# Optimization experiments

Hardware: AMD Instinct MI355X
Metric: run time of the kernel (lower is better)

The kernel has to match this reference:

```python
import jax, jax.numpy as jnp
import numpy as np

D_MODEL = 1024
N_HEADS = 16
HEAD_DIM = D_MODEL // N_HEADS


def setup_inputs() -> dict:
    key = jax.random.key(0)
    ks = jax.random.split(key, 5)
    B, L = 4, 2048
    x = jax.random.normal(ks[0], (B, L, D_MODEL), dtype=jnp.float32)
    s = 1.0 / np.sqrt(D_MODEL)
    W_qkv = jax.random.normal(ks[1], (D_MODEL, 3 * D_MODEL), dtype=jnp.float32) * s
    b_qkv = jnp.zeros((3 * D_MODEL,), dtype=jnp.float32)
    W_out = jax.random.normal(ks[2], (D_MODEL, D_MODEL), dtype=jnp.float32) * s
    b_out = jnp.zeros((D_MODEL,), dtype=jnp.float32)
    return {"x": x, "W_qkv": W_qkv, "b_qkv": b_qkv, "W_out": W_out, "b_out": b_out}


def reference(x, W_qkv, b_qkv, W_out, b_out):
    B, L, D = x.shape
    qkv = x @ W_qkv + b_qkv                      # [B, L, 3D]
    q, k, v = jnp.split(qkv, 3, axis=-1)
    def split_heads(t):
        return t.reshape(B, L, N_HEADS, HEAD_DIM).transpose(0, 2, 1, 3)  # [B,H,L,hd]
    q, k, v = split_heads(q), split_heads(k), split_heads(v)
    scale = 1.0 / np.sqrt(HEAD_DIM).astype(np.float32)
    scores = jnp.einsum('bhqd,bhkd->bhqk', q, k) * scale  # [B,H,L,L]
    causal = jnp.tril(jnp.ones((L, L), dtype=bool))       # True = keep
    scores = jnp.where(causal, scores, -jnp.inf)
    attn = jax.nn.softmax(scores, axis=-1)
    out = jnp.einsum('bhqk,bhkd->bhqd', attn, v)          # [B,H,L,hd]
    out = out.transpose(0, 2, 1, 3).reshape(B, L, D)
    return out @ W_out + b_out
```

## Files before the change

kernel.cpp:

```cpp
#include <hip/hip_runtime.h>
#include <hip/hip_bf16.h>
#include <stdint.h>

#define D_MODEL 1024
#define NH 16
#define HD 64
#define LSEQ 2048
#define BATCH 4
#define NROWS (BATCH * LSEQ)
#define SCALE_L2E 0.18033688011112042f

typedef __attribute__((ext_vector_type(8))) short s16x8;
typedef __attribute__((ext_vector_type(4))) float f32x4;
typedef __attribute__((ext_vector_type(4))) int   i32x4;

static __device__ __forceinline__ f32x4 mfma_bf16(s16x8 a, s16x8 b, f32x4 c) {
    return __builtin_amdgcn_mfma_f32_16x16x32_bf16(a, b, c, 0, 0, 0);
}

static __device__ __forceinline__ unsigned short f32_to_bf16(float f) {
    unsigned int u = __float_as_uint(f);
    u = (u + 0x7fffu + ((u >> 16) & 1u)) >> 16;
    return (unsigned short)u;
}

static __device__ __forceinline__ unsigned int cvtpk(float lo, float hi) {
    unsigned int r;
    asm("v_cvt_pk_bf16_f32 %0, %1, %2" : "=v"(r) : "v"(lo), "v"(hi));
    return r;
}

static __device__ __forceinline__ unsigned long long pack4(float a, float b,
                                                           float c, float d) {
    return (unsigned long long)cvtpk(a, b) |
           ((unsigned long long)cvtpk(c, d) << 32);
}

static __device__ __forceinline__ void gload16(const void* g, void* l) {
    __builtin_amdgcn_global_load_lds(
        (const __attribute__((address_space(1))) void*)g,
        (__attribute__((address_space(3))) void*)l, 16, 0, 0);
}


__global__ void cvt_f32_bf16(const float* __restrict__ in,
                             unsigned short* __restrict__ out, int n4) {
    int i = blockIdx.x * blockDim.x + threadIdx.x;
    if (i < n4) {
        float4 v = ((const float4*)in)[i];
        ushort4 o;
        o.x = f32_to_bf16(v.x); o.y = f32_to_bf16(v.y);
        o.z = f32_to_bf16(v.z); o.w = f32_to_bf16(v.w);
        ((ushort4*)out)[i] = o;
    }
}

__global__ __launch_bounds__(256) void transpose_cvt(
    const float* __restrict__ in, unsigned short* __restrict__ out, int K, int N) {
    __shared__ float tile[32][33];
    int n0 = blockIdx.x * 32, k0 = blockIdx.y * 32;
    int tx = threadIdx.x & 31, ty = threadIdx.x >> 5;
    #pragma unroll
    for (int i = 0; i < 4; i++) {
        int k = ty + i * 8;
        tile[k][tx] = in[(size_t)(k0 + k) * N + (n0 + tx)];
    }
    __syncthreads();
    #pragma unroll
    for (int i = 0; i < 4; i++) {
        int n = ty + i * 8;
        out[(size_t)(n0 + n) * K + (k0 + tx)] = f32_to_bf16(tile[tx][n]);
    }
}


__global__ __launch_bounds__(512, 2) void gemm256_qkv(
    const unsigned short* __restrict__ A,
    const unsigned short* __restrict__ Bt,
    const float* __restrict__ bias,
    unsigned short* __restrict__ q_buf, unsigned short* __restrict__ k_buf,
    unsigned short* __restrict__ vT) {
    extern __shared__ float4 smv[];
    char* sm = (char*)smv;
    const int K = 1024, NT = 16;
    const int tid = threadIdx.x;
    const int lane = tid & 63, w = tid >> 6;
    const int wm = w >> 2, wn = w & 3;
    const int lq = lane & 15, lk = lane >> 4;
    const int m0 = blockIdx.y * 256, n0 = blockIdx.x * 256;

    const unsigned short* GA = A + (size_t)m0 * K;
    const unsigned short* GB = Bt + (size_t)n0 * K;

    auto stage = [&](const unsigned short* G, int mat, int t, int half) {
        char* base = sm + (t & 1) * 65536 + mat * 32768 + half * 16384;
        const unsigned short* g0 = G + (size_t)(half * 128) * K + t * 64;
        #pragma unroll
        for (int j = 0; j < 2; j++) {
            int c = j * 512 + tid;
            int row = c >> 3, cc = c & 7;
            int cg = cc ^ (row & 7);
            gload16(g0 + (size_t)row * K + cg * 8,
                    base + (j * 512 + w * 64) * 16);
        }
    };
    auto lda = [&](int buf, int mf, int ks) -> s16x8 {
        int byte = (((mf * 16 + lq) * 128 + ks * 64 + lk * 16)) ^ ((lq & 7) << 4);
        return *(const s16x8*)(sm + buf * 65536 + wm * 16384 + byte);
    };
    auto ldb = [&](int buf, int nf, int ks) -> s16x8 {
        int byte = ((((wn & 1) * 64 + nf * 16 + lq) * 128 + ks * 64 + lk * 16)) ^
                   ((lq & 7) << 4);
        return *(const s16x8*)(sm + buf * 65536 + 32768 + (wn >> 1) * 16384 + byte);
    };

    f32x4 acc[8][4];
    #pragma unroll
    for (int m = 0; m < 8; m++)
        #pragma unroll
        for (int n = 0; n < 4; n++)
            #pragma unroll
            for (int r = 0; r < 4; r++) acc[m][n][r] = 0.f;

    stage(GA, 0, 0, 0); stage(GA, 0, 0, 1); stage(GB, 1, 0, 0); stage(GB, 1, 0, 1);
    stage(GA, 0, 1, 0); stage(GA, 0, 1, 1); stage(GB, 1, 1, 0);
    asm volatile("s_waitcnt vmcnt(6)" ::: "memory");
    __builtin_amdgcn_s_barrier();

    s16x8 alo[4][2], ahi[4][2], blo[2][2], bhi[2][2];
    for (int t = 0; t < NT; t++) {
        const int buf = t & 1;
        #pragma unroll
        for (int mf = 0; mf < 4; mf++)
            #pragma unroll
            for (int ks = 0; ks < 2; ks++) alo[mf][ks] = lda(buf, mf, ks);
        #pragma unroll
        for (int nf = 0; nf < 2; nf++)
            #pragma unroll
            for (int ks = 0; ks < 2; ks++) blo[nf][ks] = ldb(buf, nf, ks);
        if (t + 1 < NT) stage(GB, 1, t + 1, 1);
        __builtin_amdgcn_s_barrier();
        asm volatile("s_waitcnt lgkmcnt(0)" ::: "memory");
        __builtin_amdgcn_s_setprio(1);
        #pragma unroll
        for (int mf = 0; mf < 4; mf++)
            #pragma unroll
            for (int nf = 0; nf < 2; nf++)
                #pragma unroll
                for (int ks = 0; ks < 2; ks++)
                    acc[mf][nf] = mfma_bf16(alo[mf][ks], blo[nf][ks], acc[mf][nf]);
        __builtin_amdgcn_s_setprio(0);
        __builtin_amdgcn_s_barrier();
        #pragma unroll
        for (int nf = 0; nf < 2; nf++)
            #pragma unroll
            for (int ks = 0; ks < 2; ks++) bhi[nf][ks] = ldb(buf, 2 + nf, ks);
        __builtin_amdgcn_s_barrier();
        asm volatile("s_waitcnt lgkmcnt(0)" ::: "memory");
        __builtin_amdgcn_s_setprio(1);
        #pragma unroll
        for (int mf = 0; mf < 4; mf++)
            #pragma unroll
            for (int nf = 0; nf < 2; nf++)
                #pragma unroll
                for (int ks = 0; ks < 2; ks++)
                    acc[mf][2 + nf] = mfma_bf16(alo[mf][ks], bhi[nf][ks], acc[mf][2 + nf]);
        __builtin_amdgcn_s_setprio(0);
        __builtin_amdgcn_s_barrier();
        #pragma unroll
        for (int mf = 0; mf < 4; mf++)
            #pragma unroll
            for (int ks = 0; ks < 2; ks++) ahi[mf][ks] = lda(buf, 4 + mf, ks);
        if (t + 2 < NT) stage(GB, 1, t + 2, 0);
        __builtin_amdgcn_s_barrier();
        asm volatile("s_waitcnt lgkmcnt(0)" ::: "memory");
        __builtin_amdgcn_s_setprio(1);
        #pragma unroll
        for (int mf = 0; mf < 4; mf++)
            #pragma unroll
            for (int nf = 0; nf < 2; nf++)
                #pragma unroll
                for (int ks = 0; ks < 2; ks++)
                    acc[4 + mf][nf] = mfma_bf16(ahi[mf][ks], blo[nf][ks], acc[4 + mf][nf]);
        __builtin_amdgcn_s_setprio(0);
        __builtin_amdgcn_s_barrier();
        if (t + 2 < NT) { stage(GA, 0, t + 2, 0); stage(GA, 0, t + 2, 1); }
        __builtin_amdgcn_s_barrier();
        asm volatile("s_waitcnt lgkmcnt(0)" ::: "memory");
        __builtin_amdgcn_s_setprio(1);
        #pragma unroll
        for (int mf = 0; mf < 4; mf++)
            #pragma unroll
            for (int nf = 0; nf < 2; nf++)
                #pragma unroll
                for (int ks = 0; ks < 2; ks++)
                    acc[4 + mf][2 + nf] = mfma_bf16(ahi[mf][ks], bhi[nf][ks], acc[4 + mf][2 + nf]);
        __builtin_amdgcn_s_setprio(0);
        if (t + 2 < NT) {
            asm volatile("s_waitcnt vmcnt(6)" ::: "memory");
        } else if (t + 1 < NT) {
            asm volatile("s_waitcnt vmcnt(0)" ::: "memory");
        }
        __builtin_amdgcn_s_barrier();
    }

    const int rowb = m0 + wm * 128 + lk * 4;
    const int colb = n0 + wn * 64 + lq;
    if (n0 < 1024) {
        #pragma unroll
        for (int mf = 0; mf < 8; mf++) {
            int row = rowb + mf * 16;
            #pragma unroll
            for (int nf = 0; nf < 4; nf++) {
                int col = colb + nf * 16;
                float bv = bias[col];
                #pragma unroll
                for (int r = 0; r < 4; r++)
                    q_buf[(size_t)(row + r) * 1024 + col] =
                        f32_to_bf16((acc[mf][nf][r] + bv) * SCALE_L2E);
            }
        }
    } else if (n0 < 2048) {
        #pragma unroll
        for (int mf = 0; mf < 8; mf++) {
            int row = rowb + mf * 16;
            #pragma unroll
            for (int nf = 0; nf < 4; nf++) {
                int col = colb + nf * 16;
                float bv = bias[col];
                #pragma unroll
                for (int r = 0; r < 4; r++)
                    k_buf[(size_t)(row + r) * 1024 + (col - 1024)] =
                        f32_to_bf16(acc[mf][nf][r] + bv);
            }
        }
    } else {
        #pragma unroll
        for (int mf = 0; mf < 8; mf++) {
            int row = rowb + mf * 16;
            int bb = row >> 11, pos = row & 2047;
            #pragma unroll
            for (int nf = 0; nf < 4; nf++) {
                int col = colb + nf * 16;
                int dg = col - 2048;
                float bv = bias[col];
                unsigned long long pk =
                    pack4(acc[mf][nf][0] + bv, acc[mf][nf][1] + bv,
                          acc[mf][nf][2] + bv, acc[mf][nf][3] + bv);
                *(unsigned long long*)(vT +
                    ((size_t)((bb * 16 + (dg >> 6)) * 64 + (dg & 63))) * 2048 + pos) = pk;
            }
        }
    }
}


__global__ __launch_bounds__(256) void gemm_bf16_f32(
    const unsigned short* __restrict__ A,
    const unsigned short* __restrict__ Bt,
    const float* __restrict__ bias,
    float* __restrict__ C, int M, int N, int K) {
    __shared__ __align__(16) unsigned short As[2][128][32];
    __shared__ __align__(16) unsigned short Bs[2][128][32];

    const int tid = threadIdx.x;
    const int m0 = blockIdx.y * 128;
    const int n0 = blockIdx.x * 128;
    const int lane = tid & 63, w4 = tid >> 6;
    const int wr = w4 >> 1, wc = w4 & 1;
    const int lq = lane & 15, lk = lane >> 4;

    const int srow = lane >> 2;
    const int sk = (lane & 3) * 8;
    const unsigned short* ap = A  + (size_t)(m0 + w4 * 16 + srow) * K + sk;
    const unsigned short* bp = Bt + (size_t)(n0 + w4 * 16 + srow) * K + sk;

    f32x4 acc[4][4];
    #pragma unroll
    for (int m = 0; m < 4; m++)
        #pragma unroll
        for (int n = 0; n < 4; n++)
            #pragma unroll
            for (int r = 0; r < 4; r++) acc[m][n][r] = 0.f;

    gload16(ap,                  &As[0][w4 * 16][0]);
    gload16(ap + (size_t)64 * K, &As[0][64 + w4 * 16][0]);
    gload16(bp,                  &Bs[0][w4 * 16][0]);
    gload16(bp + (size_t)64 * K, &Bs[0][64 + w4 * 16][0]);
    __syncthreads();

    int buf = 0;
    for (int k0 = 0; k0 < K; k0 += 32) {
        if (k0 + 32 < K) {
            const unsigned short* ap2 = ap + k0 + 32;
            const unsigned short* bp2 = bp + k0 + 32;
            gload16(ap2,                  &As[buf ^ 1][w4 * 16][0]);
            gload16(ap2 + (size_t)64 * K, &As[buf ^ 1][64 + w4 * 16][0]);
            gload16(bp2,                  &Bs[buf ^ 1][w4 * 16][0]);
            gload16(bp2 + (size_t)64 * K, &Bs[buf ^ 1][64 + w4 * 16][0]);
        }
        s16x8 af[4], bfr[4];
        #pragma unroll
        for (int m = 0; m < 4; m++)
            af[m] = *(const s16x8*)(&As[buf][wr * 64 + m * 16 + lq][lk * 8]);
        #pragma unroll
        for (int n = 0; n < 4; n++)
            bfr[n] = *(const s16x8*)(&Bs[buf][wc * 64 + n * 16 + lq][lk * 8]);
        #pragma unroll
        for (int m = 0; m < 4; m++)
            #pragma unroll
            for (int n = 0; n < 4; n++)
                acc[m][n] = mfma_bf16(af[m], bfr[n], acc[m][n]);
        __syncthreads();
        buf ^= 1;
    }

    #pragma unroll
    for (int m = 0; m < 4; m++) {
        int row = m0 + wr * 64 + m * 16 + lk * 4;
        #pragma unroll
        for (int n = 0; n < 4; n++) {
            int col = n0 + wc * 64 + n * 16 + lq;
            float bv = bias[col];
            #pragma unroll
            for (int r = 0; r < 4; r++)
                C[(size_t)(row + r) * N + col] = acc[m][n][r] + bv;
        }
    }
}


__global__ __launch_bounds__(256) void attn_kernel(
    const unsigned short* __restrict__ q_buf,
    const unsigned short* __restrict__ k_buf,
    const unsigned short* __restrict__ vT,
    unsigned short* __restrict__ out) {
    __shared__ __align__(16) char lds[24576];
    char* Ks = lds;
    char* Vs = lds + 8192;

    const int bh = blockIdx.y;
    const int b = bh >> 4, h = bh & 15;
    const int qb0 = ((int)gridDim.x - 1 - (int)blockIdx.x) * 64;
    const int tid = threadIdx.x, lane = tid & 63, w = tid >> 6;
    const int lq = lane & 15, lk = lane >> 4;
    char* Pw = lds + 16384 + w * 2048;

    const int q_g = qb0 + w * 16 + lq;
    const unsigned short* qp = q_buf + ((size_t)b * LSEQ + q_g) * 1024 + h * 64;
    const s16x8 qf0 = *(const s16x8*)(qp + lk * 8);
    const s16x8 qf1 = *(const s16x8*)(qp + 32 + lk * 8);

    const int srow = tid >> 3, sch = tid & 7;
    const int sby0 = (srow * 128 + sch * 16) ^ ((srow & 7) << 4);
    const int sby1 = ((srow + 32) * 128 + sch * 16) ^ ((srow & 7) << 4);
    const int swzA = (lq & 7) << 4;

    const unsigned short* kp =
        k_buf + (size_t)b * LSEQ * 1024 + h * 64 + (size_t)srow * 1024 + sch * 8;
    const unsigned short* vp =
        vT + (size_t)bh * 64 * 2048 + (size_t)srow * 2048 + sch * 8;

    float m_r = -1e30f, l_r = 0.f;
    f32x4 o[4];
    #pragma unroll
    for (int n = 0; n < 4; n++)
        #pragma unroll
        for (int r = 0; r < 4; r++) o[n][r] = 0.f;

    const int nkv = qb0 / 64 + 1;

    i32x4 r0 = *(const i32x4*)kp;
    i32x4 r1 = *(const i32x4*)(kp + (size_t)32 * 1024);
    i32x4 r2 = *(const i32x4*)vp;
    i32x4 r3 = *(const i32x4*)(vp + (size_t)32 * 2048);

    for (int kvb = 0; kvb < nkv; kvb++) {
        *(i32x4*)(Ks + sby0) = r0;
        *(i32x4*)(Ks + sby1) = r1;
        *(i32x4*)(Vs + sby0) = r2;
        *(i32x4*)(Vs + sby1) = r3;
        __syncthreads();
        if (kvb + 1 < nkv) {
            kp += 64 * 1024;
            vp += 64;
            r0 = *(const i32x4*)kp;
            r1 = *(const i32x4*)(kp + (size_t)32 * 1024);
            r2 = *(const i32x4*)vp;
            r3 = *(const i32x4*)(vp + (size_t)32 * 2048);
        }

        f32x4 sT[4];
        #pragma unroll
        for (int n = 0; n < 4; n++)
            #pragma unroll
            for (int r = 0; r < 4; r++) sT[n][r] = 0.f;
        __builtin_amdgcn_s_setprio(1);
        #pragma unroll
        for (int n = 0; n < 4; n++) {
            const int rb = (n * 16 + lq) * 128;
            s16x8 a0 = *(const s16x8*)(Ks + ((rb + lk * 16) ^ swzA));
            s16x8 a1 = *(const s16x8*)(Ks + ((rb + 64 + lk * 16) ^ swzA));
            sT[n] = mfma_bf16(a0, qf0, sT[n]);
            sT[n] = mfma_bf16(a1, qf1, sT[n]);
        }
        __builtin_amdgcn_s_setprio(0);
        if (kvb == nkv - 1) {
            const int kv0 = kvb * 64;
            #pragma unroll
            for (int n = 0; n < 4; n++)
                #pragma unroll
                for (int r = 0; r < 4; r++)
                    if (kv0 + n * 16 + lk * 4 + r > q_g) sT[n][r] = -1e30f;
        }

        float mx = sT[0][0];
        #pragma unroll
        for (int n = 0; n < 4; n++)
            #pragma unroll
            for (int r = 0; r < 4; r++) mx = fmaxf(mx, sT[n][r]);
        mx = fmaxf(mx, __shfl_xor(mx, 16, 64));
        mx = fmaxf(mx, __shfl_xor(mx, 32, 64));
        if (!__all(mx <= m_r + 8.f)) {
            const float mnew = fmaxf(m_r, mx);
            const float corr = __builtin_amdgcn_exp2f(m_r - mnew);
            m_r = mnew;
            l_r *= corr;
            #pragma unroll
            for (int n = 0; n < 4; n++)
                #pragma unroll
                for (int r = 0; r < 4; r++) o[n][r] *= corr;
        }
        float sum = 0.f;
        unsigned long long pk[4];
        #pragma unroll
        for (int n = 0; n < 4; n++) {
            float p0 = __builtin_amdgcn_exp2f(sT[n][0] - m_r);
            float p1 = __builtin_amdgcn_exp2f(sT[n][1] - m_r);
            float p2 = __builtin_amdgcn_exp2f(sT[n][2] - m_r);
            float p3 = __builtin_amdgcn_exp2f(sT[n][3] - m_r);
            sum += (p0 + p1) + (p2 + p3);
            pk[n] = pack4(p0, p1, p2, p3);
        }
        l_r += sum;

        #pragma unroll
        for (int n = 0; n < 4; n++)
            *(unsigned long long*)(Pw + ((lq * 128 + n * 32 + lk * 8) ^ swzA)) = pk[n];
        asm volatile("s_waitcnt lgkmcnt(0)" ::: "memory");

        __builtin_amdgcn_s_setprio(1);
        #pragma unroll
        for (int kk = 0; kk < 2; kk++) {
            s16x8 pb = *(const s16x8*)(Pw + ((lq * 128 + kk * 64 + lk * 16) ^ swzA));
            #pragma unroll
            for (int n = 0; n < 4; n++) {
                s16x8 vf = *(const s16x8*)(Vs +
                    (((n * 16 + lq) * 128 + kk * 64 + lk * 16) ^ swzA));
                o[n] = mfma_bf16(vf, pb, o[n]);
            }
        }
        __builtin_amdgcn_s_setprio(0);
        asm volatile("s_barrier" ::: "memory");
    }

    l_r += __shfl_xor(l_r, 16, 64);
    l_r += __shfl_xor(l_r, 32, 64);
    const float inv = 1.f / l_r;
    unsigned short* op = out + ((size_t)b * LSEQ + q_g) * 1024 + h * 64;
    #pragma unroll
    for (int n = 0; n < 4; n++) {
        unsigned long long pkv = pack4(o[n][0] * inv, o[n][1] * inv,
                                       o[n][2] * inv, o[n][3] * inv);
        *(unsigned long long*)(op + n * 16 + lk * 4) = pkv;
    }
}


extern "C" void kernel_launch(void* const* d_in, const int* in_sizes, int n_in,
                              void* d_out, int out_size, void* d_ws, size_t ws_size,
                              hipStream_t stream) {
    const float* x     = (const float*)d_in[0];
    const float* W_qkv = (const float*)d_in[1];
    const float* b_qkv = (const float*)d_in[2];
    const float* W_out = (const float*)d_in[3];
    const float* b_out = (const float*)d_in[4];
    float* out = (float*)d_out;

    char* p = (char*)d_ws;
    unsigned short* x_bf   = (unsigned short*)p; p += (size_t)NROWS * D_MODEL * 2;
    unsigned short* wqkv_t = (unsigned short*)p; p += (size_t)3 * D_MODEL * D_MODEL * 2;
    unsigned short* wout_t = (unsigned short*)p; p += (size_t)D_MODEL * D_MODEL * 2;
    unsigned short* q_buf  = (unsigned short*)p; p += (size_t)NROWS * D_MODEL * 2;
    unsigned short* k_buf  = (unsigned short*)p; p += (size_t)NROWS * D_MODEL * 2;
    unsigned short* vT     = (unsigned short*)p; p += (size_t)NROWS * D_MODEL * 2;
    unsigned short* attn   = (unsigned short*)p;

    hipFuncSetAttribute((const void*)gemm256_qkv,
                        hipFuncAttributeMaxDynamicSharedMemorySize, 131072);

    int n4 = NROWS * D_MODEL / 4;
    hipLaunchKernelGGL(cvt_f32_bf16, dim3((n4 + 255) / 256), dim3(256), 0, stream,
                       x, x_bf, n4);
    hipLaunchKernelGGL(transpose_cvt, dim3(3 * D_MODEL / 32, D_MODEL / 32), dim3(256),
                       0, stream, W_qkv, wqkv_t, D_MODEL, 3 * D_MODEL);
    hipLaunchKernelGGL(transpose_cvt, dim3(D_MODEL / 32, D_MODEL / 32), dim3(256),
                       0, stream, W_out, wout_t, D_MODEL, D_MODEL);
    hipLaunchKernelGGL(gemm256_qkv, dim3(3 * D_MODEL / 256, NROWS / 256),
                       dim3(512), 131072, stream, x_bf, wqkv_t, b_qkv,
                       q_buf, k_buf, vT);
    hipLaunchKernelGGL(attn_kernel, dim3(LSEQ / 64, BATCH * NH), dim3(256), 0, stream,
                       q_buf, k_buf, vT, attn);
    hipLaunchKernelGGL(gemm_bf16_f32, dim3(D_MODEL / 128, NROWS / 128),
                       dim3(256), 0, stream, attn, wout_t, b_out, out,
                       NROWS, D_MODEL, D_MODEL);
}
```

Baseline: 318.0 us.

## Pair mirrored causal query blocks per workgroup to balance attention work

Each attention workgroup now handles two query blocks, pj and 31-pj, sharing the same K/V tiles in LDS. The combined KV length is the same for every block, which removes the causal triangle's load imbalance and halves the number of K/V tile loads for the paired rows. It also adds launch_bounds occupancy hint 4 and a larger LDS footprint. The cost is roughly double the accumulator registers per thread and fewer, longer workgroups (1024 instead of 2048).

```diff
diff --git a/kernel.cpp b/kernel.cpp
--- a/kernel.cpp
+++ b/kernel.cpp
@@ -13,6 +13,9 @@
 typedef __attribute__((ext_vector_type(8))) short s16x8;
 typedef __attribute__((ext_vector_type(4))) float f32x4;
 typedef __attribute__((ext_vector_type(4))) int   i32x4;
+
+struct TrueT  { static constexpr bool value = true;  };
+struct FalseT { static constexpr bool value = false; };
 
 static __device__ __forceinline__ f32x4 mfma_bf16(s16x8 a, s16x8 b, f32x4 c) {
     return __builtin_amdgcn_mfma_f32_16x16x32_bf16(a, b, c, 0, 0, 0);
@@ -330,26 +333,34 @@
 }
 
 
-__global__ __launch_bounds__(256) void attn_kernel(
+__global__ __launch_bounds__(256, 4) void attn_kernel(
     const unsigned short* __restrict__ q_buf,
     const unsigned short* __restrict__ k_buf,
     const unsigned short* __restrict__ vT,
     unsigned short* __restrict__ out) {
-    __shared__ __align__(16) char lds[24576];
+    __shared__ __align__(16) char lds[32768];
     char* Ks = lds;
     char* Vs = lds + 8192;
 
-    const int bh = blockIdx.y;
+    const int bid = blockIdx.x;
+    const int bh = bid & 63;
+    const int pj = bid >> 6;
     const int b = bh >> 4, h = bh & 15;
-    const int qb0 = ((int)gridDim.x - 1 - (int)blockIdx.x) * 64;
     const int tid = threadIdx.x, lane = tid & 63, w = tid >> 6;
     const int lq = lane & 15, lk = lane >> 4;
-    char* Pw = lds + 16384 + w * 2048;
-
-    const int q_g = qb0 + w * 16 + lq;
-    const unsigned short* qp = q_buf + ((size_t)b * LSEQ + q_g) * 1024 + h * 64;
-    const s16x8 qf0 = *(const s16x8*)(qp + lk * 8);
-    const s16x8 qf1 = *(const s16x8*)(qp + 32 + lk * 8);
+    char* PwA = lds + 16384 + w * 2048;
+    char* PwB = lds + 24576 + w * 2048;
+
+    const int nA = pj + 1, nB = 32 - pj;
+    const int qgA = pj * 64 + w * 16 + lq;
+    const int qgB = (31 - pj) * 64 + w * 16 + lq;
+
+    const unsigned short* qpA = q_buf + ((size_t)b * LSEQ + qgA) * 1024 + h * 64;
+    const unsigned short* qpB = q_buf + ((size_t)b * LSEQ + qgB) * 1024 + h * 64;
+    const s16x8 qA0 = *(const s16x8*)(qpA + lk * 8);
+    const s16x8 qA1 = *(const s16x8*)(qpA + 32 + lk * 8);
+    const s16x8 qB0 = *(const s16x8*)(qpB + lk * 8);
+    const s16x8 qB1 = *(const s16x8*)(qpB + 32 + lk * 8);
 
     const int srow = tid >> 3, sch = tid & 7;
     const int sby0 = (srow * 128 + sch * 16) ^ ((srow & 7) << 4);
@@ -361,27 +372,25 @@
     const unsigned short* vp =
         vT + (size_t)bh * 64 * 2048 + (size_t)srow * 2048 + sch * 8;
 
-    float m_r = -1e30f, l_r = 0.f;
-    f32x4 o[4];
+    float mA = -1e30f, lA = 0.f, mB = -1e30f, lB = 0.f;
+    f32x4 oA[4], oB[4];
     #pragma unroll
     for (int n = 0; n < 4; n++)
         #pragma unroll
-        for (int r = 0; r < 4; r++) o[n][r] = 0.f;
-
-    const int nkv = qb0 / 64 + 1;
+        for (int r = 0; r < 4; r++) { oA[n][r] = 0.f; oB[n][r] = 0.f; }
 
     i32x4 r0 = *(const i32x4*)kp;
     i32x4 r1 = *(const i32x4*)(kp + (size_t)32 * 1024);
     i32x4 r2 = *(const i32x4*)vp;
     i32x4 r3 = *(const i32x4*)(vp + (size_t)32 * 2048);
 
-    for (int kvb = 0; kvb < nkv; kvb++) {
+    for (int kvb = 0; kvb < nB; kvb++) {
         *(i32x4*)(Ks + sby0) = r0;
         *(i32x4*)(Ks + sby1) = r1;
         *(i32x4*)(Vs + sby0) = r2;
         *(i32x4*)(Vs + sby1) = r3;
         __syncthreads();
-        if (kvb + 1 < nkv) {
+        if (kvb + 1 < nB) {
             kp += 64 * 1024;
             vp += 64;
             r0 = *(const i32x4*)kp;
@@ -390,89 +399,147 @@
             r3 = *(const i32x4*)(vp + (size_t)32 * 2048);
         }
 
-        f32x4 sT[4];
-        #pragma unroll
-        for (int n = 0; n < 4; n++)
-            #pragma unroll
-            for (int r = 0; r < 4; r++) sT[n][r] = 0.f;
-        __builtin_amdgcn_s_setprio(1);
-        #pragma unroll
-        for (int n = 0; n < 4; n++) {
-            const int rb = (n * 16 + lq) * 128;
-            s16x8 a0 = *(const s16x8*)(Ks + ((rb + lk * 16) ^ swzA));
-            s16x8 a1 = *(const s16x8*)(Ks + ((rb + 64 + lk * 16) ^ swzA));
-            sT[n] = mfma_bf16(a0, qf0, sT[n]);
-            sT[n] = mfma_bf16(a1, qf1, sT[n]);
-        }
-        __builtin_amdgcn_s_setprio(0);
-        if (kvb == nkv - 1) {
+        auto tile = [&](auto doa_t) {
+            constexpr bool DOA = decltype(doa_t)::value;
+            f32x4 sA[4], sB[4];
+            #pragma unroll
+            for (int n = 0; n < 4; n++)
+                #pragma unroll
+                for (int r = 0; r < 4; r++) {
+                    sB[n][r] = 0.f;
+                    if (DOA) sA[n][r] = 0.f;
+                }
+            __builtin_amdgcn_s_setprio(1);
+            #pragma unroll
+            for (int n = 0; n < 4; n++) {
+                const int rb = (n * 16 + lq) * 128;
+                s16x8 a0 = *(const s16x8*)(Ks + ((rb + lk * 16) ^ swzA));
+                s16x8 a1 = *(const s16x8*)(Ks + ((rb + 64 + lk * 16) ^ swzA));
+                sB[n] = mfma_bf16(a0, qB0, sB[n]);
+                sB[n] = mfma_bf16(a1, qB1, sB[n]);
+                if (DOA) {
+                    sA[n] = mfma_bf16(a0, qA0, sA[n]);
+                    sA[n] = mfma_bf16(a1, qA1, sA[n]);
+                }
+            }
+            __builtin_amdgcn_s_setprio(0);
             const int kv0 = kvb * 64;
-            #pragma unroll
-            for (int n = 0; n < 4; n++)
-                #pragma unroll
-                for (int r = 0; r < 4; r++)
-                    if (kv0 + n * 16 + lk * 4 + r > q_g) sT[n][r] = -1e30f;
-        }
-
-        float mx = sT[0][0];
-        #pragma unroll
-        for (int n = 0; n < 4; n++)
-            #pragma unroll
-            for (int r = 0; r < 4; r++) mx = fmaxf(mx, sT[n][r]);
-        mx = fmaxf(mx, __shfl_xor(mx, 16, 64));
-        mx = fmaxf(mx, __shfl_xor(mx, 32, 64));
-        if (!__all(mx <= m_r + 8.f)) {
-            const float mnew = fmaxf(m_r, mx);
-            const float corr = __builtin_amdgcn_exp2f(m_r - mnew);
-            m_r = mnew;
-            l_r *= corr;
-            #pragma unroll
-            for (int n = 0; n < 4; n++)
-                #pragma unroll
-                for (int r = 0; r < 4; r++) o[n][r] *= corr;
-        }
-        float sum = 0.f;
-        unsigned long long pk[4];
-        #pragma unroll
-        for (int n = 0; n < 4; n++) {
-            float p0 = __builtin_amdgcn_exp2f(sT[n][0] - m_r);
-            float p1 = __builtin_amdgcn_exp2f(sT[n][1] - m_r);
-            float p2 = __builtin_amdgcn_exp2f(sT[n][2] - m_r);
-            float p3 = __builtin_amdgcn_exp2f(sT[n][3] - m_r);
-            sum += (p0 + p1) + (p2 + p3);
-            pk[n] = pack4(p0, p1, p2, p3);
-        }
-        l_r += sum;
-
-        #pragma unroll
-        for (int n = 0; n < 4; n++)
-            *(unsigned long long*)(Pw + ((lq * 128 + n * 32 + lk * 8) ^ swzA)) = pk[n];
-        asm volatile("s_waitcnt lgkmcnt(0)" ::: "memory");
-
-        __builtin_amdgcn_s_setprio(1);
-        #pragma unroll
-        for (int kk = 0; kk < 2; kk++) {
-            s16x8 pb = *(const s16x8*)(Pw + ((lq * 128 + kk * 64 + lk * 16) ^ swzA));
+            if (kvb == nB - 1) {
+                #pragma unroll
+                for (int n = 0; n < 4; n++)
+                    #pragma unroll
+                    for (int r = 0; r < 4; r++)
+                        if (kv0 + n * 16 + lk * 4 + r > qgB) sB[n][r] = -1e30f;
+            }
+            if (DOA && kvb == nA - 1) {
+                #pragma unroll
+                for (int n = 0; n < 4; n++)
+                    #pragma unroll
+                    for (int r = 0; r < 4; r++)
+                        if (kv0 + n * 16 + lk * 4 + r > qgA) sA[n][r] = -1e30f;
+            }
+            unsigned long long pkB[4], pkA[4];
+            {
+                float mx = sB[0][0];
+                #pragma unroll
+                for (int n = 0; n < 4; n++)
+                    #pragma unroll
+                    for (int r = 0; r < 4; r++) mx = fmaxf(mx, sB[n][r]);
+                mx = fmaxf(mx, __shfl_xor(mx, 16, 64));
+                mx = fmaxf(mx, __shfl_xor(mx, 32, 64));
+                if (!__all(mx <= mB + 8.f)) {
+                    const float mnew = fmaxf(mB, mx);
+                    const float corr = __builtin_amdgcn_exp2f(mB - mnew);
+                    mB = mnew; lB *= corr;
+                    #pragma unroll
+                    for (int n = 0; n < 4; n++)
+                        #pragma unroll
+                        for (int r = 0; r < 4; r++) oB[n][r] *= corr;
+                }
+                float sum = 0.f;
+                #pragma unroll
+                for (int n = 0; n < 4; n++) {
+                    float p0 = __builtin_amdgcn_exp2f(sB[n][0] - mB);
+                    float p1 = __builtin_amdgcn_exp2f(sB[n][1] - mB);
+                    float p2 = __builtin_amdgcn_exp2f(sB[n][2] - mB);
+                    float p3 = __builtin_amdgcn_exp2f(sB[n][3] - mB);
+                    sum += (p0 + p1) + (p2 + p3);
+                    pkB[n] = pack4(p0, p1, p2, p3);
+                }
+                lB += sum;
+            }
+            if (DOA) {
+                float mx = sA[0][0];
+                #pragma unroll
+                for (int n = 0; n < 4; n++)
+                    #pragma unroll
+                    for (int r = 0; r < 4; r++) mx = fmaxf(mx, sA[n][r]);
+                mx = fmaxf(mx, __shfl_xor(mx, 16, 64));
+                mx = fmaxf(mx, __shfl_xor(mx, 32, 64));
+                if (!__all(mx <= mA + 8.f)) {
+                    const float mnew = fmaxf(mA, mx);
+                    const float corr = __builtin_amdgcn_exp2f(mA - mnew);
+                    mA = mnew; lA *= corr;
+                    #pragma unroll
+                    for (int n = 0; n < 4; n++)
+                        #pragma unroll
+                        for (int r = 0; r < 4; r++) oA[n][r] *= corr;
+                }
+                float sum = 0.f;
+                #pragma unroll
+                for (int n = 0; n < 4; n++) {
+                    float p0 = __builtin_amdgcn_exp2f(sA[n][0] - mA);
+                    float p1 = __builtin_amdgcn_exp2f(sA[n][1] - mA);
+                    float p2 = __builtin_amdgcn_exp2f(sA[n][2] - mA);
+                    float p3 = __builtin_amdgcn_exp2f(sA[n][3] - mA);
+                    sum += (p0 + p1) + (p2 + p3);
+                    pkA[n] = pack4(p0, p1, p2, p3);
+                }
+                lA += sum;
+            }
             #pragma unroll
             for (int n = 0; n < 4; n++) {
-                s16x8 vf = *(const s16x8*)(Vs +
-                    (((n * 16 + lq) * 128 + kk * 64 + lk * 16) ^ swzA));
-                o[n] = mfma_bf16(vf, pb, o[n]);
-            }
-        }
-        __builtin_amdgcn_s_setprio(0);
+                const int pb_off = (lq * 128 + n * 32 + lk * 8) ^ swzA;
+                *(unsigned long long*)(PwB + pb_off) = pkB[n];
+                if (DOA) *(unsigned long long*)(PwA + pb_off) = pkA[n];
+            }
+            asm volatile("s_waitcnt lgkmcnt(0)" ::: "memory");
+            __builtin_amdgcn_s_setprio(1);
+            #pragma unroll
+            for (int kk = 0; kk < 2; kk++) {
+                const int p_off = (lq * 128 + kk * 64 + lk * 16) ^ swzA;
+                s16x8 pbB = *(const s16x8*)(PwB + p_off);
+                s16x8 pbA;
+                if (DOA) pbA = *(const s16x8*)(PwA + p_off);
+                #pragma unroll
+                for (int n = 0; n < 4; n++) {
+                    s16x8 vf = *(const s16x8*)(Vs +
+                        (((n * 16 + lq) * 128 + kk * 64 + lk * 16) ^ swzA));
+                    oB[n] = mfma_bf16(vf, pbB, oB[n]);
+                    if (DOA) oA[n] = mfma_bf16(vf, pbA, oA[n]);
+                }
+            }
+            __builtin_amdgcn_s_setprio(0);
+        };
+        if (kvb < nA) tile(TrueT{}); else tile(FalseT{});
+
         asm volatile("s_barrier" ::: "memory");
     }
 
-    l_r += __shfl_xor(l_r, 16, 64);
-    l_r += __shfl_xor(l_r, 32, 64);
-    const float inv = 1.f / l_r;
-    unsigned short* op = out + ((size_t)b * LSEQ + q_g) * 1024 + h * 64;
+    lB += __shfl_xor(lB, 16, 64);
+    lB += __shfl_xor(lB, 32, 64);
+    lA += __shfl_xor(lA, 16, 64);
+    lA += __shfl_xor(lA, 32, 64);
+    const float invB = 1.f / lB;
+    const float invA = 1.f / lA;
+    unsigned short* opB = out + ((size_t)b * LSEQ + qgB) * 1024 + h * 64;
+    unsigned short* opA = out + ((size_t)b * LSEQ + qgA) * 1024 + h * 64;
     #pragma unroll
     for (int n = 0; n < 4; n++) {
-        unsigned long long pkv = pack4(o[n][0] * inv, o[n][1] * inv,
-                                       o[n][2] * inv, o[n][3] * inv);
-        *(unsigned long long*)(op + n * 16 + lk * 4) = pkv;
+        *(unsigned long long*)(opB + n * 16 + lk * 4) =
+            pack4(oB[n][0] * invB, oB[n][1] * invB, oB[n][2] * invB, oB[n][3] * invB);
+        *(unsigned long long*)(opA + n * 16 + lk * 4) =
+            pack4(oA[n][0] * invA, oA[n][1] * invA, oA[n][2] * invA, oA[n][3] * invA);
     }
 }
 
@@ -509,7 +576,7 @@
     hipLaunchKernelGGL(gemm256_qkv, dim3(3 * D_MODEL / 256, NROWS / 256),
                        dim3(512), 131072, stream, x_bf, wqkv_t, b_qkv,
                        q_buf, k_buf, vT);
-    hipLaunchKernelGGL(attn_kernel, dim3(LSEQ / 64, BATCH * NH), dim3(256), 0, stream,
+    hipLaunchKernelGGL(attn_kernel, dim3(16 * 64), dim3(256), 0, stream,
                        q_buf, k_buf, vT, attn);
     hipLaunchKernelGGL(gemm_bf16_f32, dim3(D_MODEL / 128, NROWS / 128),
                        dim3(256), 0, stream, attn, wout_t, b_out, out,
```

Result: slower. 417.4 us (+31.3%).
